# Kernel optimization log

Hardware: AMD Instinct MI355X
Metric: run time of the kernel (lower is better)

Reference implementation:

```python
import jax, jax.numpy as jnp
import numpy as np

N_QUBITS = 16
N_BLOCKS = 8
N_ADDR_QUBITS = 4  # (8).bit_length() -> min(n_qubits, bit_length)
N_HEADS = 16


def setup_inputs() -> dict:
    key = jax.random.key(0)
    ks = jax.random.split(key, 9)
    B, S, D, M, J, Q = 4, 2048, 1024, 2048, N_BLOCKS, N_QUBITS
    s = lambda d: 1.0 / np.sqrt(d)
    return {
        "query": jax.random.normal(ks[0], (B, S, D), jnp.float32),
        "W_addr": jax.random.normal(ks[1], (D, Q), jnp.float32) * s(D),
        "b_addr": jnp.zeros((Q,), jnp.float32),
        "memory": jax.random.normal(ks[2], (J, M), jnp.float32),
        "W_out": jax.random.normal(ks[3], (M, D), jnp.float32) * s(M),
        "b_out": jnp.zeros((D,), jnp.float32),
        "Wq": jax.random.normal(ks[4], (D, D), jnp.float32) * s(D),
        "bq": jnp.zeros((D,), jnp.float32),
        "Wk": jax.random.normal(ks[5], (D, D), jnp.float32) * s(D),
        "bk": jnp.zeros((D,), jnp.float32),
        "Wv": jax.random.normal(ks[6], (D, D), jnp.float32) * s(D),
        "bv": jnp.zeros((D,), jnp.float32),
        "Wo": jax.random.normal(ks[7], (D, D), jnp.float32) * s(D),
        "bo": jnp.zeros((D,), jnp.float32),
    }


def _address_weights(query, W_addr, b_addr):
    # Deterministic expectation of the per-token quantum register loop:
    # RX(theta) applied iff theta > 0 -> P(measure 1) = sin^2(theta/2), else 0.
    theta = query @ W_addr + b_addr                      # [B,S,Q]
    p1 = jnp.where(theta > 0, jnp.sin(theta * 0.5) ** 2, 0.0)
    p = p1[..., :N_ADDR_QUBITS]                          # only bit_length(J) qubits used
    bits = ((jnp.arange(N_BLOCKS)[:, None] >> jnp.arange(N_ADDR_QUBITS)[None, :]) & 1
            ).astype(query.dtype)                        # [J, Qa]
    # score[b,s,j] = sum_q [ bits*p + (1-bits)*(1-p) ]
    scores = jnp.einsum("bsq,jq->bsj", p, bits) + jnp.einsum("bsq,jq->bsj", 1.0 - p, 1.0 - bits)
    return jax.nn.softmax(scores, axis=-1)               # [B,S,J]


def reference(query, W_addr, b_addr, memory, W_out, b_out,
              Wq, bq, Wk, bk, Wv, bv, Wo, bo):
    addr = _address_weights(query, W_addr, b_addr)       # [B,S,J]
    mem_read = jnp.einsum("bsj,jm->bsm", addr, memory)   # [B,S,M]
    out = mem_read @ W_out + b_out                       # [B,S,D]

    # quantum_attention(q=k=v=out): multi-head self-attention
    B, S, D = out.shape
    hd = D // N_HEADS
    q = (out @ Wq + bq).reshape(B, S, N_HEADS, hd)
    k = (out @ Wk + bk).reshape(B, S, N_HEADS, hd)
    v = (out @ Wv + bv).reshape(B, S, N_HEADS, hd)
    att = jax.nn.softmax(jnp.einsum("bihd,bjhd->bhij", q, k) / np.sqrt(hd), axis=-1)
    ctx = jnp.einsum("bhij,bjhd->bihd", att, v).reshape(B, S, D)
    return ctx @ Wo + bo
```

## Files before the change

kernel.cpp:

```cpp
#include <hip/hip_runtime.h>

#define B_ 4
#define S_ 2048
#define D_ 1024
#define M_ 2048
#define J_ 8
#define H_ 16
#define HD_ 64
#define BH_ 64

typedef __attribute__((ext_vector_type(8))) short short8;
typedef __attribute__((ext_vector_type(4))) float f32x4;
typedef __attribute__((ext_vector_type(16))) float f32x16;

static __device__ __forceinline__ unsigned short f2bf(float x) {
  unsigned u = __float_as_uint(x);
  u = u + 0x7fffu + ((u >> 16) & 1u);
  return (unsigned short)(u >> 16);
}

static __device__ __forceinline__ unsigned cvtpk(float lo, float hi) {
  unsigned r;
  asm("v_cvt_pk_bf16_f32 %0, %1, %2" : "=v"(r) : "v"(lo), "v"(hi));
  return r;
}

__global__ __launch_bounds__(256) void k_mw_part(const float* __restrict__ memory,
                                                 const float* __restrict__ W_out,
                                                 float* __restrict__ part) {
  int nc = blockIdx.x >> 4, ks = blockIdx.x & 15;
  int t = threadIdx.x;
  int n = nc * 64 + (t & 63);
  int sub = t >> 6;
  int k0 = ks * 128 + sub * 32;
  float acc[J_];
#pragma unroll
  for (int j = 0; j < J_; ++j) acc[j] = 0.f;
  for (int k = k0; k < k0 + 32; ++k) {
    float wv = W_out[(size_t)k * D_ + n];
#pragma unroll
    for (int j = 0; j < J_; ++j) acc[j] += memory[j * M_ + k] * wv;
  }
  __shared__ float p4[4][J_][64];
#pragma unroll
  for (int j = 0; j < J_; ++j) p4[sub][j][t & 63] = acc[j];
  __syncthreads();
  if (t < 64) {
#pragma unroll
    for (int j = 0; j < J_; ++j)
      part[((size_t)ks * J_ + j) * D_ + nc * 64 + t] =
          p4[0][j][t] + p4[1][j][t] + p4[2][j][t] + p4[3][j][t];
  }
}

__global__ __launch_bounds__(256) void k_mw_red(const float* __restrict__ part,
                                                const float* __restrict__ b_out,
                                                float* __restrict__ G) {
  int id = blockIdx.x * 256 + threadIdx.x;
  int j = id >> 10, n = id & 1023;
  if (j < 8) {
    float s = 0.f;
#pragma unroll
    for (int ks = 0; ks < 16; ++ks) s += part[((size_t)ks * J_ + j) * D_ + n];
    G[j * D_ + n] = s;
  } else {
    G[8 * D_ + n] = b_out[n];
  }
}

__global__ __launch_bounds__(256) void k_mwq_part(const float* __restrict__ G,
                                                  const float* __restrict__ Wq,
                                                  const float* __restrict__ Wk,
                                                  const float* __restrict__ Wv,
                                                  float* __restrict__ partq) {
  int wi = blockIdx.x >> 6;
  int r = blockIdx.x & 63;
  int nc = r & 15, ks = r >> 4;
  const float* W = wi == 0 ? Wq : (wi == 1 ? Wk : Wv);
  int t = threadIdx.x;
  int n = nc * 64 + (t & 63);
  int sub = t >> 6;
  int k0 = ks * 256 + sub * 64;
  float acc[9];
#pragma unroll
  for (int j = 0; j < 9; ++j) acc[j] = 0.f;
  for (int k = k0; k < k0 + 64; ++k) {
    float wv = W[(size_t)k * D_ + n];
#pragma unroll
    for (int j = 0; j < 9; ++j) acc[j] += G[j * D_ + k] * wv;
  }
  __shared__ float p4[4][9][64];
#pragma unroll
  for (int j = 0; j < 9; ++j) p4[sub][j][t & 63] = acc[j];
  __syncthreads();
  if (t < 64) {
#pragma unroll
    for (int j = 0; j < 9; ++j)
      partq[(((size_t)wi * 4 + ks) * 9 + j) * D_ + nc * 64 + t] =
          p4[0][j][t] + p4[1][j][t] + p4[2][j][t] + p4[3][j][t];
  }
}

__global__ __launch_bounds__(256) void k_mwq_red(const float* __restrict__ partq,
                                                 float* __restrict__ Hq,
                                                 float* __restrict__ Hk,
                                                 float* __restrict__ Hv) {
  int id = blockIdx.x * 256 + threadIdx.x;
  int wi = id / 9216;
  int rem = id - wi * 9216;
  int j = rem >> 10, n = rem & 1023;
  float s = 0.f;
#pragma unroll
  for (int ks = 0; ks < 4; ++ks)
    s += partq[(((size_t)wi * 4 + ks) * 9 + j) * D_ + n];
  float* Hh = wi == 0 ? Hq : (wi == 1 ? Hk : Hv);
  Hh[j * D_ + n] = s;
}

__global__ __launch_bounds__(256) void k_wot(const float* __restrict__ Wo,
                                             unsigned short* __restrict__ WoT) {
  int kt = blockIdx.x, nt = blockIdx.y;
  int t = threadIdx.x;
  __shared__ float tl[64][65];
  int r = t >> 6, c = t & 63;
#pragma unroll
  for (int i = 0; i < 16; ++i) {
    int row = i * 4 + r;
    tl[row][c] = Wo[(size_t)(kt * 64 + row) * D_ + nt * 64 + c];
  }
  __syncthreads();
#pragma unroll
  for (int i = 0; i < 16; ++i) {
    int nrow = i * 4 + r;
    WoT[(size_t)(nt * 64 + nrow) * D_ + kt * 64 + c] = f2bf(tl[c][nrow]);
  }
}

__global__ __launch_bounds__(256) void k_qkv(
    const float* __restrict__ query, const float* __restrict__ W_addr,
    const float* __restrict__ b_addr, const float* __restrict__ Hq,
    const float* __restrict__ Hk, const float* __restrict__ Hv,
    const float* __restrict__ bq, const float* __restrict__ bk,
    const float* __restrict__ bv, unsigned short* __restrict__ Qg,
    unsigned short* __restrict__ Kg, unsigned short* __restrict__ Vg) {
  int w = threadIdx.x >> 6, l = threadIdx.x & 63;
  int tk = blockIdx.x * 4 + w;
  int b = tk >> 11, s = tk & (S_ - 1);
  const float* qrow = query + (size_t)tk * D_;
  float th0 = 0.f, th1 = 0.f, th2 = 0.f, th3 = 0.f;
#pragma unroll
  for (int e = 0; e < 4; ++e) {
    float4 qv = *(const float4*)(qrow + l * 16 + e * 4);
    float xs[4] = {qv.x, qv.y, qv.z, qv.w};
#pragma unroll
    for (int kk = 0; kk < 4; ++kk) {
      float4 wr = *(const float4*)(W_addr + (size_t)(l * 16 + e * 4 + kk) * 16);
      th0 += xs[kk] * wr.x;
      th1 += xs[kk] * wr.y;
      th2 += xs[kk] * wr.z;
      th3 += xs[kk] * wr.w;
    }
  }
#pragma unroll
  for (int off = 32; off; off >>= 1) {
    th0 += __shfl_xor(th0, off);
    th1 += __shfl_xor(th1, off);
    th2 += __shfl_xor(th2, off);
    th3 += __shfl_xor(th3, off);
  }
  float thv[4] = {th0 + b_addr[0], th1 + b_addr[1], th2 + b_addr[2],
                  th3 + b_addr[3]};
  float p[4];
#pragma unroll
  for (int q = 0; q < 4; ++q) {
    float sh = __sinf(thv[q] * 0.5f);
    p[q] = thv[q] > 0.f ? sh * sh : 0.f;
  }
  float sc[8];
  float mx = -1e30f;
#pragma unroll
  for (int j = 0; j < 8; ++j) {
    float v = 0.f;
#pragma unroll
    for (int q = 0; q < 4; ++q) v += ((j >> q) & 1) ? p[q] : 1.f - p[q];
    sc[j] = v;
    mx = fmaxf(mx, v);
  }
  float sum = 0.f;
#pragma unroll
  for (int j = 0; j < 8; ++j) {
    sc[j] = __expf(sc[j] - mx);
    sum += sc[j];
  }
  float inv = 1.f / sum;
  float a[8];
#pragma unroll
  for (int j = 0; j < 8; ++j) a[j] = sc[j] * inv;

  const float* Hs[3] = {Hq, Hk, Hv};
  const float* bs[3] = {bq, bk, bv};
  unsigned short* os[3] = {Qg, Kg, Vg};
#pragma unroll
  for (int k = 0; k < 4; ++k) {
    int n0 = k * 256 + l * 4;
    int hh = n0 >> 6, d = n0 & 63;
    size_t obase = ((size_t)(b * H_ + hh) * S_ + s) * HD_ + d;
#pragma unroll
    for (int wi = 0; wi < 3; ++wi) {
      const float* Hh = Hs[wi];
      float4 accv = *(const float4*)(Hh + 8 * D_ + n0);
      float4 bias = *(const float4*)(bs[wi] + n0);
      accv.x += bias.x; accv.y += bias.y; accv.z += bias.z; accv.w += bias.w;
#pragma unroll
      for (int j = 0; j < 8; ++j) {
        float4 hv = *(const float4*)(Hh + j * D_ + n0);
        accv.x += a[j] * hv.x;
        accv.y += a[j] * hv.y;
        accv.z += a[j] * hv.z;
        accv.w += a[j] * hv.w;
      }
      uint2 pk;
      pk.x = (unsigned)f2bf(accv.x) | ((unsigned)f2bf(accv.y) << 16);
      pk.y = (unsigned)f2bf(accv.z) | ((unsigned)f2bf(accv.w) << 16);
      *(uint2*)(os[wi] + obase) = pk;
    }
  }
}

__global__ __launch_bounds__(256) void k_vt(const unsigned short* __restrict__ Vg,
                                            unsigned short* __restrict__ Vtg) {
  int st = blockIdx.x & 31, bh = blockIdx.x >> 5;
  int t = threadIdx.x;
  __shared__ unsigned short tl[64][65];
  int rr = t >> 3, c8 = t & 7;
#pragma unroll
  for (int p = 0; p < 2; ++p) {
    int s = p * 32 + rr;
    uint4 v = *(const uint4*)(Vg + ((size_t)bh * S_ + st * 64 + s) * HD_ + c8 * 8);
    const unsigned short* pv = (const unsigned short*)&v;
#pragma unroll
    for (int j = 0; j < 8; ++j) tl[s][c8 * 8 + j] = pv[j];
  }
  __syncthreads();
#pragma unroll
  for (int p = 0; p < 2; ++p) {
    int d = p * 32 + rr;
    unsigned short o[8];
#pragma unroll
    for (int j = 0; j < 8; ++j) o[j] = tl[c8 * 8 + j][d];
    *(uint4*)(Vtg + ((size_t)bh * HD_ + d) * S_ + st * 64 + c8 * 8) = *(const uint4*)o;
  }
}

__global__ __launch_bounds__(512, 4) void k_attn(
    const unsigned short* __restrict__ Qg, const unsigned short* __restrict__ Kg,
    const unsigned short* __restrict__ Vtg, unsigned short* __restrict__ ctxg) {
  int id = blockIdx.x;
  int xcd = id & 7, kk_ = id >> 3;
  int bh = xcd * 8 + (kk_ >> 3);
  int qt = kk_ & 7;
  int t = threadIdx.x;
  int w = t >> 6, l = t & 63;
  int q31 = l & 31, h = l >> 5;

  __shared__ __align__(16) unsigned short lds[16384];

  int q0 = qt * 256 + w * 32;
  const unsigned short* qp = Qg + ((size_t)bh * S_ + q0 + q31) * HD_;
  short8 qf0 = *(const short8*)(qp + 0 + h * 8);
  short8 qf1 = *(const short8*)(qp + 16 + h * 8);
  short8 qf2 = *(const short8*)(qp + 32 + h * 8);
  short8 qf3 = *(const short8*)(qp + 48 + h * 8);

  f32x16 accO0 = {}, accO1 = {};
  float m = -1e30f, lsum = 0.f;

  int srow = t >> 3, sc8 = t & 7;
  const unsigned short* kgb = Kg + (size_t)bh * S_ * HD_;
  const unsigned short* vtb = Vtg + (size_t)bh * HD_ * S_;
  int di = srow * 64 + ((sc8 * 8) ^ ((srow & 7) << 3));

  uint4 rK = *(const uint4*)(kgb + (size_t)srow * HD_ + sc8 * 8);
  uint4 rV = *(const uint4*)(vtb + (size_t)srow * S_ + sc8 * 8);
  *(uint4*)(lds + di) = rK;
  *(uint4*)(lds + 4096 + di) = rV;
  __syncthreads();

  for (int it = 0; it < 32; ++it) {
    int kv0 = it * 64;
    unsigned short* sK = lds + (it & 1) * 8192;
    unsigned short* sVt = sK + 4096;
    if (it < 31) {
      rK = *(const uint4*)(kgb + (size_t)(kv0 + 64 + srow) * HD_ + sc8 * 8);
      rV = *(const uint4*)(vtb + (size_t)srow * S_ + kv0 + 64 + sc8 * 8);
    }

    f32x16 accS0 = {}, accS1 = {};
    __builtin_amdgcn_s_setprio(1);
#pragma unroll
    for (int ds = 0; ds < 4; ++ds) {
      short8 qq = ds == 0 ? qf0 : ds == 1 ? qf1 : ds == 2 ? qf2 : qf3;
      {
        int row = q31;
        int g = (ds * 2 + h) ^ (row & 7);
        short8 kf = *(const short8*)(sK + row * 64 + g * 8);
        accS0 = __builtin_amdgcn_mfma_f32_32x32x16_bf16(kf, qq, accS0, 0, 0, 0);
      }
      {
        int row = 32 + q31;
        int g = (ds * 2 + h) ^ (row & 7);
        short8 kf = *(const short8*)(sK + row * 64 + g * 8);
        accS1 = __builtin_amdgcn_mfma_f32_32x32x16_bf16(kf, qq, accS1, 0, 0, 0);
      }
    }
    __builtin_amdgcn_s_setprio(0);

    float mxv = accS0[0];
#pragma unroll
    for (int r = 1; r < 16; ++r) mxv = fmaxf(mxv, accS0[r]);
#pragma unroll
    for (int r = 0; r < 16; ++r) mxv = fmaxf(mxv, accS1[r]);
    mxv = fmaxf(mxv, __shfl_xor(mxv, 32));
    float pm = mxv * 0.125f;
    if (__ballot(pm > m + 8.f)) {
      float mn = fmaxf(m, pm);
      float scl = __builtin_exp2f((m - mn) * 1.44269504f);
#pragma unroll
      for (int r = 0; r < 16; ++r) {
        accO0[r] *= scl;
        accO1[r] *= scl;
      }
      lsum *= scl;
      m = mn;
    }
    const float K1 = 0.125f * 1.44269504f;
    float m2 = m * 1.44269504f;
    float ts = 0.f;
#pragma unroll
    for (int r = 0; r < 16; ++r) {
      float p0 = __builtin_exp2f(accS0[r] * K1 - m2);
      float p1 = __builtin_exp2f(accS1[r] * K1 - m2);
      accS0[r] = p0;
      accS1[r] = p1;
      ts += p0 + p1;
    }
    ts += __shfl_xor(ts, 32);
    lsum += ts;

    short8 pb[4];
#pragma unroll
    for (int ks = 0; ks < 4; ++ks) {
      const int r0 = 8 * (ks & 1);
      float v0, v1, v2, v3, v4, v5, v6, v7;
      if (ks < 2) {
        v0 = accS0[r0 + 0]; v1 = accS0[r0 + 1]; v2 = accS0[r0 + 2]; v3 = accS0[r0 + 3];
        v4 = accS0[r0 + 4]; v5 = accS0[r0 + 5]; v6 = accS0[r0 + 6]; v7 = accS0[r0 + 7];
      } else {
        v0 = accS1[r0 + 0]; v1 = accS1[r0 + 1]; v2 = accS1[r0 + 2]; v3 = accS1[r0 + 3];
        v4 = accS1[r0 + 4]; v5 = accS1[r0 + 5]; v6 = accS1[r0 + 6]; v7 = accS1[r0 + 7];
      }
      unsigned X0 = cvtpk(v0, v1), X1 = cvtpk(v2, v3);
      unsigned Y0 = cvtpk(v4, v5), Y1 = cvtpk(v6, v7);
      unsigned tX0 = __shfl_xor(X0, 32), tX1 = __shfl_xor(X1, 32);
      unsigned tY0 = __shfl_xor(Y0, 32), tY1 = __shfl_xor(Y1, 32);
      union { unsigned u[4]; short8 s8; } uu;
      uu.u[0] = h ? tY0 : X0;
      uu.u[1] = h ? tY1 : X1;
      uu.u[2] = h ? Y0 : tX0;
      uu.u[3] = h ? Y1 : tX1;
      pb[ks] = uu.s8;
    }

    __builtin_amdgcn_s_setprio(1);
    {
      int row = q31;
      int rs = row & 7;
#pragma unroll
      for (int ks = 0; ks < 4; ++ks) {
        int g = (ks * 2 + h) ^ rs;
        short8 vf = *(const short8*)(sVt + row * 64 + g * 8);
        accO0 = __builtin_amdgcn_mfma_f32_32x32x16_bf16(vf, pb[ks], accO0, 0, 0, 0);
      }
    }
    {
      int row = 32 + q31;
      int rs = row & 7;
#pragma unroll
      for (int ks = 0; ks < 4; ++ks) {
        int g = (ks * 2 + h) ^ rs;
        short8 vf = *(const short8*)(sVt + row * 64 + g * 8);
        accO1 = __builtin_amdgcn_mfma_f32_32x32x16_bf16(vf, pb[ks], accO1, 0, 0, 0);
      }
    }
    __builtin_amdgcn_s_setprio(0);

    if (it < 31) {
      unsigned short* dK = lds + ((it + 1) & 1) * 8192;
      *(uint4*)(dK + di) = rK;
      *(uint4*)(dK + 4096 + di) = rV;
    }
    __syncthreads();
  }

  float inv = 1.f / lsum;
  unsigned short* sO = lds + w * 2048;
#pragma unroll
  for (int r = 0; r < 16; ++r) {
    int dl = (r & 3) + 8 * (r >> 2) + 4 * h;
    int swz = (q31 & 7) << 3;
    sO[q31 * 64 + (dl ^ swz)] = f2bf(accO0[r] * inv);
    sO[q31 * 64 + ((32 + dl) ^ swz)] = f2bf(accO1[r] * inv);
  }
  __syncthreads();
  int b = bh >> 4, head = bh & 15;
  int rr = l & 31, hh = l >> 5;
  unsigned short* orow = ctxg + ((size_t)(b * S_ + q0 + rr)) * D_ + head * HD_;
#pragma unroll
  for (int j = 0; j < 4; ++j) {
    int g = hh * 4 + j;
    uint4 vv = *(const uint4*)(sO + rr * 64 + ((g ^ (rr & 7)) * 8));
    *(uint4*)(orow + g * 8) = vv;
  }
}

__global__ __launch_bounds__(256) void k_out(const unsigned short* __restrict__ Ag,
                                             const unsigned short* __restrict__ Btg,
                                             const float* __restrict__ bo,
                                             float* __restrict__ out) {
  int mt = blockIdx.x;
  int nt = blockIdx.y;
  int t = threadIdx.x;
  int w = t >> 6, l = t & 63;
  int l15 = l & 15, l4 = l >> 4;
  int wr = w >> 1, wc = w & 1;
  __shared__ __align__(16) unsigned short sA[128 * 64];
  __shared__ __align__(16) unsigned short sB[128 * 64];
  f32x4 acc[4][4];
#pragma unroll
  for (int mm = 0; mm < 4; ++mm)
#pragma unroll
    for (int nn = 0; nn < 4; ++nn) acc[mm][nn] = (f32x4){0.f, 0.f, 0.f, 0.f};
  int srow = t >> 3, sc8 = t & 7;
  for (int kt = 0; kt < 16; ++kt) {
    int k0 = kt * 64;
    __syncthreads();
#pragma unroll
    for (int p = 0; p < 4; ++p) {
      int row = p * 32 + srow;
      int di = row * 64 + ((sc8 * 8) ^ ((row & 7) << 3));
      *(uint4*)(sA + di) =
          *(const uint4*)(Ag + (size_t)(mt * 128 + row) * D_ + k0 + sc8 * 8);
      *(uint4*)(sB + di) =
          *(const uint4*)(Btg + (size_t)(nt * 128 + row) * D_ + k0 + sc8 * 8);
    }
    __syncthreads();
    short8 a[4][2];
#pragma unroll
    for (int mm = 0; mm < 4; ++mm) {
      int row = wr * 64 + mm * 16 + l15;
      int sw = (row & 7) << 3;
      a[mm][0] = *(const short8*)(sA + row * 64 + ((l4 * 8) ^ sw));
      a[mm][1] = *(const short8*)(sA + row * 64 + ((32 + l4 * 8) ^ sw));
    }
#pragma unroll
    for (int nn = 0; nn < 4; ++nn) {
      int row = wc * 64 + nn * 16 + l15;
      int sw = (row & 7) << 3;
      short8 b0 = *(const short8*)(sB + row * 64 + ((l4 * 8) ^ sw));
      short8 b1 = *(const short8*)(sB + row * 64 + ((32 + l4 * 8) ^ sw));
#pragma unroll
      for (int mm = 0; mm < 4; ++mm) {
        acc[mm][nn] = __builtin_amdgcn_mfma_f32_16x16x32_bf16(a[mm][0], b0, acc[mm][nn], 0, 0, 0);
        acc[mm][nn] = __builtin_amdgcn_mfma_f32_16x16x32_bf16(a[mm][1], b1, acc[mm][nn], 0, 0, 0);
      }
    }
  }
#pragma unroll
  for (int mm = 0; mm < 4; ++mm) {
#pragma unroll
    for (int r = 0; r < 4; ++r) {
      int mrow = mt * 128 + wr * 64 + mm * 16 + l4 * 4 + r;
      float* orow = out + (size_t)mrow * D_ + nt * 128 + wc * 64;
#pragma unroll
      for (int nn = 0; nn < 4; ++nn) {
        int n = nn * 16 + l15;
        orow[n] = acc[mm][nn][r] + bo[nt * 128 + wc * 64 + n];
      }
    }
  }
}

extern "C" void kernel_launch(void* const* d_in, const int* in_sizes, int n_in,
                              void* d_out, int out_size, void* d_ws, size_t ws_size,
                              hipStream_t stream) {
  const float* query = (const float*)d_in[0];
  const float* W_addr = (const float*)d_in[1];
  const float* b_addr = (const float*)d_in[2];
  const float* memory = (const float*)d_in[3];
  const float* W_out = (const float*)d_in[4];
  const float* b_out = (const float*)d_in[5];
  const float* Wq = (const float*)d_in[6];
  const float* bq = (const float*)d_in[7];
  const float* Wk = (const float*)d_in[8];
  const float* bk = (const float*)d_in[9];
  const float* Wv = (const float*)d_in[10];
  const float* bv = (const float*)d_in[11];
  const float* Wo = (const float*)d_in[12];
  const float* bo = (const float*)d_in[13];
  float* out = (float*)d_out;

  char* ws = (char*)d_ws;
  size_t off = 0;
  auto alloc = [&](size_t bytes) {
    char* p = ws + off;
    off = (off + bytes + 255) & ~(size_t)255;
    return p;
  };
  float* G = (float*)alloc(9 * D_ * sizeof(float));
  float* HqA = (float*)alloc(9 * D_ * sizeof(float));
  float* HkA = (float*)alloc(9 * D_ * sizeof(float));
  float* HvA = (float*)alloc(9 * D_ * sizeof(float));
  float* partmw = (float*)alloc(16 * J_ * D_ * sizeof(float));
  float* partq = (float*)alloc(3 * 4 * 9 * D_ * sizeof(float));
  unsigned short* WoT = (unsigned short*)alloc((size_t)D_ * D_ * 2);
  unsigned short* Vg = (unsigned short*)alloc((size_t)BH_ * S_ * HD_ * 2);
  unsigned short* Vtg = (unsigned short*)alloc((size_t)BH_ * S_ * HD_ * 2);
  unsigned short* Qg = (unsigned short*)d_out;
  unsigned short* Kg = Qg + (size_t)BH_ * S_ * HD_;
  unsigned short* ctx = Vg;

  k_mw_part<<<256, 256, 0, stream>>>(memory, W_out, partmw);
  k_mw_red<<<36, 256, 0, stream>>>(partmw, b_out, G);
  k_mwq_part<<<192, 256, 0, stream>>>(G, Wq, Wk, Wv, partq);
  k_mwq_red<<<108, 256, 0, stream>>>(partq, HqA, HkA, HvA);
  k_wot<<<dim3(16, 16), 256, 0, stream>>>(Wo, WoT);
  k_qkv<<<B_ * S_ / 4, 256, 0, stream>>>(query, W_addr, b_addr, HqA, HkA, HvA,
                                         bq, bk, bv, Qg, Kg, Vg);
  k_vt<<<BH_ * 32, 256, 0, stream>>>(Vg, Vtg);
  k_attn<<<512, 512, 0, stream>>>(Qg, Kg, Vtg, ctx);
  k_out<<<dim3(64, 8), 256, 0, stream>>>(ctx, WoT, bo, out);
}
```

Baseline: 247.7 us.

## Split attention KV range across two warp groups with LDS merge and direct-to-LDS loads

```diff
diff --git a/kernel.cpp b/kernel.cpp
--- a/kernel.cpp
+++ b/kernel.cpp
@@ -23,6 +23,12 @@
   unsigned r;
   asm("v_cvt_pk_bf16_f32 %0, %1, %2" : "=v"(r) : "v"(lo), "v"(hi));
   return r;
+}
+
+static __device__ __forceinline__ void gload16(const void* g, void* l) {
+  __builtin_amdgcn_global_load_lds(
+      (const __attribute__((address_space(1))) unsigned*)g,
+      (__attribute__((address_space(3))) unsigned*)l, 16, 0, 0);
 }
 
 __global__ __launch_bounds__(256) void k_mw_part(const float* __restrict__ memory,
@@ -256,17 +262,20 @@
     const unsigned short* __restrict__ Qg, const unsigned short* __restrict__ Kg,
     const unsigned short* __restrict__ Vtg, unsigned short* __restrict__ ctxg) {
   int id = blockIdx.x;
-  int xcd = id & 7, kk_ = id >> 3;
-  int bh = xcd * 8 + (kk_ >> 3);
-  int qt = kk_ & 7;
+  int xcd = id & 7;
+  int qt = (id >> 3) & 15;
+  int bh = xcd * 8 + (id >> 7);
   int t = threadIdx.x;
   int w = t >> 6, l = t & 63;
   int q31 = l & 31, h = l >> 5;
+  int g = w >> 2;
 
   __shared__ __align__(16) unsigned short lds[16384];
-
-  int q0 = qt * 256 + w * 32;
-  const unsigned short* qp = Qg + ((size_t)bh * S_ + q0 + q31) * HD_;
+  unsigned short* sK = lds + g * 8192;
+  unsigned short* sVt = sK + 4096;
+
+  int q0 = qt * 128;
+  const unsigned short* qp = Qg + ((size_t)bh * S_ + q0 + (w & 3) * 32 + q31) * HD_;
   short8 qf0 = *(const short8*)(qp + 0 + h * 8);
   short8 qf1 = *(const short8*)(qp + 16 + h * 8);
   short8 qf2 = *(const short8*)(qp + 32 + h * 8);
@@ -275,25 +284,23 @@
   f32x16 accO0 = {}, accO1 = {};
   float m = -1e30f, lsum = 0.f;
 
-  int srow = t >> 3, sc8 = t & 7;
   const unsigned short* kgb = Kg + (size_t)bh * S_ * HD_;
   const unsigned short* vtb = Vtg + (size_t)bh * HD_ * S_;
-  int di = srow * 64 + ((sc8 * 8) ^ ((srow & 7) << 3));
-
-  uint4 rK = *(const uint4*)(kgb + (size_t)srow * HD_ + sc8 * 8);
-  uint4 rV = *(const uint4*)(vtb + (size_t)srow * S_ + sc8 * 8);
-  *(uint4*)(lds + di) = rK;
-  *(uint4*)(lds + 4096 + di) = rV;
-  __syncthreads();
-
-  for (int it = 0; it < 32; ++it) {
-    int kv0 = it * 64;
-    unsigned short* sK = lds + (it & 1) * 8192;
-    unsigned short* sVt = sK + 4096;
-    if (it < 31) {
-      rK = *(const uint4*)(kgb + (size_t)(kv0 + 64 + srow) * HD_ + sc8 * 8);
-      rV = *(const uint4*)(vtb + (size_t)srow * S_ + kv0 + 64 + sc8 * 8);
-    }
+  int wg = w & 3;
+  int rowK = l >> 3, gsl = l & 7;
+  int srcg = gsl ^ rowK;
+
+  for (int it = 0; it < 16; ++it) {
+    int kv0 = g * 1024 + it * 64;
+    __syncthreads();
+#pragma unroll
+    for (int cc = 0; cc < 2; ++cc) {
+      int c = wg * 2 + cc;
+      int rr = c * 8 + rowK;
+      gload16(kgb + (size_t)(kv0 + rr) * HD_ + srcg * 8, sK + c * 512);
+      gload16(vtb + (size_t)rr * S_ + kv0 + srcg * 8, sVt + c * 512);
+    }
+    __syncthreads();
 
     f32x16 accS0 = {}, accS1 = {};
     __builtin_amdgcn_s_setprio(1);
@@ -302,24 +309,22 @@
       short8 qq = ds == 0 ? qf0 : ds == 1 ? qf1 : ds == 2 ? qf2 : qf3;
       {
         int row = q31;
-        int g = (ds * 2 + h) ^ (row & 7);
-        short8 kf = *(const short8*)(sK + row * 64 + g * 8);
+        int gk = (ds * 2 + h) ^ (row & 7);
+        short8 kf = *(const short8*)(sK + row * 64 + gk * 8);
         accS0 = __builtin_amdgcn_mfma_f32_32x32x16_bf16(kf, qq, accS0, 0, 0, 0);
       }
       {
         int row = 32 + q31;
-        int g = (ds * 2 + h) ^ (row & 7);
-        short8 kf = *(const short8*)(sK + row * 64 + g * 8);
+        int gk = (ds * 2 + h) ^ (row & 7);
+        short8 kf = *(const short8*)(sK + row * 64 + gk * 8);
         accS1 = __builtin_amdgcn_mfma_f32_32x32x16_bf16(kf, qq, accS1, 0, 0, 0);
       }
     }
     __builtin_amdgcn_s_setprio(0);
 
-    float mxv = accS0[0];
-#pragma unroll
-    for (int r = 1; r < 16; ++r) mxv = fmaxf(mxv, accS0[r]);
-#pragma unroll
-    for (int r = 0; r < 16; ++r) mxv = fmaxf(mxv, accS1[r]);
+    float mxv = fmaxf(accS0[0], accS1[0]);
+#pragma unroll
+    for (int r = 1; r < 16; ++r) mxv = fmaxf(mxv, fmaxf(accS0[r], accS1[r]));
     mxv = fmaxf(mxv, __shfl_xor(mxv, 32));
     float pm = mxv * 0.125f;
     if (__ballot(pm > m + 8.f)) {
@@ -361,13 +366,20 @@
       }
       unsigned X0 = cvtpk(v0, v1), X1 = cvtpk(v2, v3);
       unsigned Y0 = cvtpk(v4, v5), Y1 = cvtpk(v6, v7);
+      union { unsigned u[4]; short8 s8; } uu;
+#if __has_builtin(__builtin_amdgcn_permlane32_swap)
+      typedef __attribute__((ext_vector_type(2))) unsigned uint2v;
+      uint2v r02 = __builtin_amdgcn_permlane32_swap(X0, Y0, false, false);
+      uint2v r13 = __builtin_amdgcn_permlane32_swap(X1, Y1, false, false);
+      uu.u[0] = r02[0]; uu.u[1] = r13[0]; uu.u[2] = r02[1]; uu.u[3] = r13[1];
+#else
       unsigned tX0 = __shfl_xor(X0, 32), tX1 = __shfl_xor(X1, 32);
       unsigned tY0 = __shfl_xor(Y0, 32), tY1 = __shfl_xor(Y1, 32);
-      union { unsigned u[4]; short8 s8; } uu;
       uu.u[0] = h ? tY0 : X0;
       uu.u[1] = h ? tY1 : X1;
       uu.u[2] = h ? Y0 : tX0;
       uu.u[3] = h ? Y1 : tX1;
+#endif
       pb[ks] = uu.s8;
     }
 
@@ -377,8 +389,8 @@
       int rs = row & 7;
 #pragma unroll
       for (int ks = 0; ks < 4; ++ks) {
-        int g = (ks * 2 + h) ^ rs;
-        short8 vf = *(const short8*)(sVt + row * 64 + g * 8);
+        int gv = (ks * 2 + h) ^ rs;
+        short8 vf = *(const short8*)(sVt + row * 64 + gv * 8);
         accO0 = __builtin_amdgcn_mfma_f32_32x32x16_bf16(vf, pb[ks], accO0, 0, 0, 0);
       }
     }
@@ -387,39 +399,72 @@
       int rs = row & 7;
 #pragma unroll
       for (int ks = 0; ks < 4; ++ks) {
-        int g = (ks * 2 + h) ^ rs;
-        short8 vf = *(const short8*)(sVt + row * 64 + g * 8);
+        int gv = (ks * 2 + h) ^ rs;
+        short8 vf = *(const short8*)(sVt + row * 64 + gv * 8);
         accO1 = __builtin_amdgcn_mfma_f32_32x32x16_bf16(vf, pb[ks], accO1, 0, 0, 0);
       }
     }
     __builtin_amdgcn_s_setprio(0);
-
-    if (it < 31) {
-      unsigned short* dK = lds + ((it + 1) & 1) * 8192;
-      *(uint4*)(dK + di) = rK;
-      *(uint4*)(dK + 4096 + di) = rV;
-    }
-    __syncthreads();
-  }
-
-  float inv = 1.f / lsum;
-  unsigned short* sO = lds + w * 2048;
-#pragma unroll
-  for (int r = 0; r < 16; ++r) {
-    int dl = (r & 3) + 8 * (r >> 2) + 4 * h;
+  }
+
+  __syncthreads();
+  if (g == 1) {
+    unsigned* xO = (unsigned*)lds;
+    int base = ((w & 3) * 64 + l) * 17;
+#pragma unroll
+    for (int j = 0; j < 8; ++j) xO[base + j] = cvtpk(accO0[2 * j], accO0[2 * j + 1]);
+#pragma unroll
+    for (int j = 0; j < 8; ++j) xO[base + 8 + j] = cvtpk(accO1[2 * j], accO1[2 * j + 1]);
+    float* xml = (float*)(lds + 8704);
+    if (h == 0) {
+      xml[(w & 3) * 32 + q31] = m;
+      xml[128 + (w & 3) * 32 + q31] = lsum;
+    }
+  }
+  __syncthreads();
+  if (g == 0) {
+    unsigned* xO = (unsigned*)lds;
+    float* xml = (float*)(lds + 8704);
+    int base = (w * 64 + l) * 17;
+    float m1 = xml[w * 32 + q31], l1 = xml[128 + w * 32 + q31];
+    float mc = fmaxf(m, m1);
+    float f0 = __builtin_exp2f((m - mc) * 1.44269504f);
+    float f1 = __builtin_exp2f((m1 - mc) * 1.44269504f);
+    float inv = 1.f / (f0 * lsum + f1 * l1);
+    f0 *= inv;
+    f1 *= inv;
+#pragma unroll
+    for (int j = 0; j < 8; ++j) {
+      unsigned wd = xO[base + j];
+      accO0[2 * j] = f0 * accO0[2 * j] + f1 * __uint_as_float(wd << 16);
+      accO0[2 * j + 1] = f0 * accO0[2 * j + 1] + f1 * __uint_as_float(wd & 0xffff0000u);
+    }
+#pragma unroll
+    for (int j = 0; j < 8; ++j) {
+      unsigned wd = xO[base + 8 + j];
+      accO1[2 * j] = f0 * accO1[2 * j] + f1 * __uint_as_float(wd << 16);
+      accO1[2 * j + 1] = f0 * accO1[2 * j + 1] + f1 * __uint_as_float(wd & 0xffff0000u);
+    }
+  }
+  __syncthreads();
+  if (g == 0) {
+    int row = w * 32 + q31;
     int swz = (q31 & 7) << 3;
-    sO[q31 * 64 + (dl ^ swz)] = f2bf(accO0[r] * inv);
-    sO[q31 * 64 + ((32 + dl) ^ swz)] = f2bf(accO1[r] * inv);
+#pragma unroll
+    for (int r = 0; r < 16; ++r) {
+      int dl = (r & 3) + 8 * (r >> 2) + 4 * h;
+      lds[row * 64 + (dl ^ swz)] = f2bf(accO0[r]);
+      lds[row * 64 + ((32 + dl) ^ swz)] = f2bf(accO1[r]);
+    }
   }
   __syncthreads();
   int b = bh >> 4, head = bh & 15;
-  int rr = l & 31, hh = l >> 5;
-  unsigned short* orow = ctxg + ((size_t)(b * S_ + q0 + rr)) * D_ + head * HD_;
-#pragma unroll
-  for (int j = 0; j < 4; ++j) {
-    int g = hh * 4 + j;
-    uint4 vv = *(const uint4*)(sO + rr * 64 + ((g ^ (rr & 7)) * 8));
-    *(uint4*)(orow + g * 8) = vv;
+#pragma unroll
+  for (int j = 0; j < 2; ++j) {
+    int slot = t + j * 512;
+    int row = slot >> 3, gg = slot & 7;
+    uint4 vv = *(const uint4*)(lds + row * 64 + ((gg ^ (row & 7)) * 8));
+    *(uint4*)(ctxg + ((size_t)(b * S_ + q0 + row)) * D_ + head * HD_ + gg * 8) = vv;
   }
 }
 
@@ -537,6 +582,6 @@
   k_qkv<<<B_ * S_ / 4, 256, 0, stream>>>(query, W_addr, b_addr, HqA, HkA, HvA,
                                          bq, bk, bv, Qg, Kg, Vg);
   k_vt<<<BH_ * 32, 256, 0, stream>>>(Vg, Vtg);
-  k_attn<<<512, 512, 0, stream>>>(Qg, Kg, Vtg, ctx);
+  k_attn<<<1024, 512, 0, stream>>>(Qg, Kg, Vtg, ctx);
   k_out<<<dim3(64, 8), 256, 0, stream>>>(ctx, WoT, bo, out);
 }
```

Measured after the change: 254.1 us. +2.6%, slower.
